# Kernel tuning notes

Hardware: AMD Instinct MI355X
Metric: run time of the kernel (lower is better)

Reference implementation:

```python
import jax, jax.numpy as jnp
import numpy as np

B, D, K, NUM_CLASSES = 8192, 512, 20, 1024
EPS = 1e-12  # torch F.normalize clamp


def setup_inputs() -> dict:
    key = jax.random.key(0)
    k1, k2 = jax.random.split(key)
    batch = jax.random.normal(k1, (B, D), dtype=jnp.float32)
    labels = jax.random.randint(k2, (B,), 0, NUM_CLASSES, dtype=jnp.int64 if jax.config.jax_enable_x64 else jnp.int32)
    return {"batch": batch, "labels": labels, "k": K}


def reference(batch, labels, k):
    # L2-normalize rows (F.normalize, p=2)
    norm = jnp.maximum(jnp.linalg.norm(batch, axis=1, keepdims=True), EPS)
    x = batch / norm
    cos = x @ x.T                                   # [B, B] cosine similarity
    min_value = cos.min() - 1.0                     # scalar, computed before diag fill
    bs = cos.shape[0]
    diag = jnp.eye(bs, dtype=bool)
    cos = jnp.where(diag, min_value, cos)           # fill_diagonal_(min_value)
    # argsort(-cos)[:, :k]  ==  top-k by similarity (self excluded via diag fill)
    top_vals, top_idx = jax.lax.top_k(cos, k)       # [B, k]
    # preds = (cos + 1)/2 gathered at neighbor indices == (top_vals + 1)/2
    preds = (top_vals + 1.0) * 0.5
    true_labels = (labels[top_idx] == labels[:, None]).astype(jnp.float32)  # [B, k]
    # nn.BCELoss with mean reduction; torch clamps each log term at -100
    logp = jnp.maximum(jnp.log(preds), -100.0)
    log1mp = jnp.maximum(jnp.log1p(-preds), -100.0)
    loss = -(true_labels * logp + (1.0 - true_labels) * log1mp)
    return loss.mean()
```

## Files before the change

kernel.cpp:

```cpp
#include <hip/hip_runtime.h>
#include <hip/hip_bf16.h>

#define NROWS 8192
#define DIM   512
#define KSEL  20
#define PANEL 1024
#define NSURV 512

typedef unsigned int u32;
typedef unsigned long long u64;
typedef short bf16x8 __attribute__((ext_vector_type(8)));
typedef float f32x4 __attribute__((ext_vector_type(4)));
typedef ushort us4 __attribute__((ext_vector_type(4)));

typedef const void __attribute__((address_space(1))) as1_void;
typedef void __attribute__((address_space(3))) as3_void;

__device__ __forceinline__ void async_ld16(const ushort* g, ushort* l) {
    __builtin_amdgcn_global_load_lds((as1_void*)g, (as3_void*)l, 16, 0, 0);
}

__device__ __forceinline__ ushort f2bf(float f) {
    u32 u = __float_as_uint(f);
    return (ushort)((u + 0x7FFFu + ((u >> 16) & 1u)) >> 16);
}

__device__ __forceinline__ u32 mono16(u32 r) {
    return r ^ (0x8000u | ((r >> 15) * 0x7FFFu));
}

__global__ __launch_bounds__(256) void k_norm(const float* __restrict__ x,
                                              ushort* __restrict__ xn) {
    int lane = threadIdx.x & 63;
    int wv   = threadIdx.x >> 6;
    int row  = blockIdx.x * 4 + wv;
    const float4* xr = (const float4*)(x + (size_t)row * DIM);
    float4 a = xr[2 * lane];
    float4 b = xr[2 * lane + 1];
    float ss = a.x*a.x + a.y*a.y + a.z*a.z + a.w*a.w
             + b.x*b.x + b.y*b.y + b.z*b.z + b.w*b.w;
    #pragma unroll
    for (int off = 32; off; off >>= 1) ss += __shfl_xor(ss, off);
    float sc = 1.0f / fmaxf(sqrtf(ss), 1e-12f);
    float v[8] = {a.x*sc, a.y*sc, a.z*sc, a.w*sc, b.x*sc, b.y*sc, b.z*sc, b.w*sc};
    union { ushort u[8]; uint4 q; } o;
    #pragma unroll
    for (int i = 0; i < 8; ++i) o.u[i] = f2bf(v[i]);
    *(uint4*)(xn + (size_t)row * DIM + lane * 8) = o.q;
}

template<bool TRI>
__global__ __launch_bounds__(256) void k_gemm(const ushort* __restrict__ xn,
                                              ushort* __restrict__ C,
                                              ushort* __restrict__ M,
                                              int row0) {
    __shared__ ushort lA[128 * 64];
    __shared__ ushort lB[128 * 64];
    int tid  = threadIdx.x;
    int lane = tid & 63, wv = tid >> 6;
    int wr = wv >> 1, wc = wv & 1;
    int q = lane >> 4, m = lane & 15;
    int bx, by;
    if (TRI) {
        int t = blockIdx.x;
        by = (int)((sqrtf(8.0f * (float)t + 1.0f) - 1.0f) * 0.5f);
        while ((by + 1) * (by + 2) / 2 <= t) ++by;
        while (by * (by + 1) / 2 > t) --by;
        bx = t - by * (by + 1) / 2;
    } else {
        bx = blockIdx.x; by = blockIdx.y;
    }
    int grow0 = row0 + by * 128;
    int gcol0 = bx * 128;
    f32x4 acc[4][4] = {};

    int lr = lane >> 3;
    int lc = lane & 7;
    for (int kc = 0; kc < 8; ++kc) {
        #pragma unroll
        for (int t = 0; t < 4; ++t) {
            int rb  = wv * 32 + t * 8;
            int r   = rb + lr;
            int fch = lc ^ (r & 7);
            async_ld16(xn + (size_t)(grow0 + r) * DIM + kc * 64 + fch * 8, &lA[rb * 64]);
            async_ld16(xn + (size_t)(gcol0 + r) * DIM + kc * 64 + fch * 8, &lB[rb * 64]);
        }
        __syncthreads();
        #pragma unroll
        for (int s = 0; s < 2; ++s) {
            bf16x8 af[4], bfr[4];
            #pragma unroll
            for (int i = 0; i < 4; ++i) {
                int ra = wr * 64 + i * 16 + m;
                af[i]  = *(const bf16x8*)&lA[ra * 64 + (((s * 4 + q) ^ (ra & 7)) * 8)];
                int rb2 = wc * 64 + i * 16 + m;
                bfr[i] = *(const bf16x8*)&lB[rb2 * 64 + (((s * 4 + q) ^ (rb2 & 7)) * 8)];
            }
            #pragma unroll
            for (int i = 0; i < 4; ++i)
                #pragma unroll
                for (int j = 0; j < 4; ++j)
                    acc[i][j] = __builtin_amdgcn_mfma_f32_16x16x32_bf16(af[i], bfr[j], acc[i][j], 0, 0, 0);
        }
        __syncthreads();
    }
    u32 cmk[4] = {0, 0, 0, 0};
    #pragma unroll
    for (int i = 0; i < 4; ++i) {
        u32 rmk[4] = {0, 0, 0, 0};
        #pragma unroll
        for (int j = 0; j < 4; ++j) {
            int c  = gcol0 + wc * 64 + j * 16 + m;
            int rb = by * 128 + wr * 64 + i * 16 + q * 4;
            ushort sv[4];
            #pragma unroll
            for (int reg = 0; reg < 4; ++reg) {
                int rl  = rb + reg;
                int grw = row0 + rl;
                ushort b = f2bf(acc[i][j][reg]);
                sv[reg] = (grw == c) ? (ushort)0xC040 : b;
                C[(size_t)rl * NROWS + c] = sv[reg];
                u32 kk = mono16((u32)sv[reg]);
                rmk[reg] = max(rmk[reg], kk);
                cmk[j]   = max(cmk[j], kk);
            }
            if (TRI && bx != by) {
                us4 pk4 = { sv[0], sv[1], sv[2], sv[3] };
                *(us4*)&C[(size_t)c * NROWS + rb] = pk4;
            }
        }
        #pragma unroll
        for (int reg = 0; reg < 4; ++reg) {
            u32 k = rmk[reg];
            k = max(k, (u32)__shfl_xor((int)k, 1));
            k = max(k, (u32)__shfl_xor((int)k, 2));
            k = max(k, (u32)__shfl_xor((int)k, 4));
            k = max(k, (u32)__shfl_xor((int)k, 8));
            if (m == 0) {
                int grw = row0 + by * 128 + wr * 64 + i * 16 + q * 4 + reg;
                M[(size_t)grw * 128 + bx * 2 + wc] = (ushort)k;
            }
        }
    }
    if (TRI && bx != by) {
        #pragma unroll
        for (int j = 0; j < 4; ++j) {
            u32 k = cmk[j];
            k = max(k, (u32)__shfl_xor((int)k, 16));
            k = max(k, (u32)__shfl_xor((int)k, 32));
            if (q == 0) {
                int gc = gcol0 + wc * 64 + j * 16 + m;
                M[(size_t)gc * 128 + by * 2 + wr] = (ushort)k;
            }
        }
    }
}

__global__ __launch_bounds__(256) void k_select(const ushort* __restrict__ C,
                                                const ushort* __restrict__ M,
                                                const int* __restrict__ labels,
                                                int row0,
                                                float* __restrict__ partials) {
    __shared__ u32 s_surv[4][NSURV];
    __shared__ u32 s_cnt[4];
    int lane = threadIdx.x & 63;
    int wv   = threadIdx.x >> 6;
    int prow = blockIdx.x * 4 + wv;
    int grow = row0 + prow;
    const ushort* rowC = C + (size_t)prow * NROWS;

    if (lane == 0) s_cnt[wv] = 0;
    __syncthreads();

    u32 pm  = *(const u32*)&M[(size_t)grow * 128 + 2 * lane];
    u32 klo = pm & 0xFFFFu, khi = pm >> 16;

    u32 T = 0;
    #pragma unroll
    for (int b = 15; b >= 0; --b) {
        u32 cand = T | (1u << b);
        int c = __popcll(__ballot(klo >= cand)) + __popcll(__ballot(khi >= cand));
        if (c >= KSEL) T = cand;
    }

    u64 rm0 = __ballot(klo >= T);
    u64 rm1 = __ballot(khi >= T);
    int nseg = __popcll(rm0) + __popcll(rm1);
    int sub = lane & 7, grp = lane >> 3;

    while (nseg > 0) {
        int ms[4] = {-1, -1, -1, -1};
        #pragma unroll
        for (int t = 0; t < 4; ++t) {
            #pragma unroll
            for (int g = 0; g < 8; ++g) {
                int seg = -1;
                if (rm0) { int b = __builtin_ctzll(rm0); seg = 2 * b;     rm0 &= rm0 - 1; }
                else if (rm1) { int b = __builtin_ctzll(rm1); seg = 2 * b + 1; rm1 &= rm1 - 1; }
                if (grp == g) ms[t] = seg;
            }
        }
        uint4 vv[4];
        #pragma unroll
        for (int t = 0; t < 4; ++t) {
            if (ms[t] >= 0) vv[t] = *(const uint4*)(rowC + ms[t] * 64 + sub * 8);
        }
        #pragma unroll
        for (int t = 0; t < 4; ++t) {
            if (ms[t] < 0) continue;
            u32 wds[4] = { vv[t].x, vv[t].y, vv[t].z, vv[t].w };
            u32 cbase = (u32)(ms[t] * 64 + sub * 8);
            #pragma unroll
            for (int h = 0; h < 4; ++h) {
                u32 w  = wds[h];
                u32 kA = mono16(w & 0xFFFFu);
                u32 kB = mono16(w >> 16);
                if (kA >= T) { u32 p = atomicAdd(&s_cnt[wv], 1u); if (p < NSURV) s_surv[wv][p] = (kA << 16) | (cbase + 2u * h); }
                if (kB >= T) { u32 p = atomicAdd(&s_cnt[wv], 1u); if (p < NSURV) s_surv[wv][p] = (kB << 16) | (cbase + 2u * h + 1u); }
            }
        }
        nseg -= 32;
    }

    u32 cnt = min(s_cnt[wv], (u32)NSURV);
    u32 g[8];
    #pragma unroll
    for (int j = 0; j < 8; ++j) {
        u32 idx = (u32)lane + (u32)j * 64u;
        g[j] = (idx < cnt) ? s_surv[wv][idx] : 0u;
    }

    u32 V = 0;
    #pragma unroll
    for (int b = 15; b >= 0; --b) {
        u32 cand = V | (1u << b);
        int c = 0;
        #pragma unroll
        for (int j = 0; j < 8; ++j)
            c += __popcll(__ballot((g[j] >> 16) >= cand));
        if (c >= KSEL) V = cand;
    }
    int cgt = 0, ceq = 0;
    #pragma unroll
    for (int j = 0; j < 8; ++j) {
        cgt += __popcll(__ballot(g[j] != 0 && (g[j] >> 16) > V));
        ceq += __popcll(__ballot(g[j] != 0 && (g[j] >> 16) == V));
    }
    int need = KSEL - cgt;
    bool all_ties = (ceq == need);

    int mylab = labels[grow];
    float loss = 0.0f;
    #pragma unroll
    for (int j = 0; j < 8; ++j) {
        u32 key = g[j] >> 16, col = g[j] & 0xFFFFu;
        if (g[j] != 0 && (key > V || (all_ties && key == V))) {
            u32 raw = (key & 0x8000u) ? (key ^ 0x8000u) : (key ^ 0xFFFFu);
            float v = __uint_as_float(raw << 16);
            float p = (v + 1.0f) * 0.5f;
            bool tm = (labels[col] == mylab);
            loss -= tm ? fmaxf(logf(p), -100.0f) : fmaxf(log1pf(-p), -100.0f);
        }
    }
    if (!all_ties) {
        for (int r = 0; r < need; ++r) {
            u32 best = 0;
            #pragma unroll
            for (int j = 0; j < 8; ++j) {
                u32 c2 = (g[j] != 0 && (g[j] >> 16) == V) ? ((g[j] & 0xFFFFu) + 1u) : 0u;
                best = max(best, c2);
            }
            #pragma unroll
            for (int off = 32; off; off >>= 1) best = max(best, (u32)__shfl_xor((int)best, off));
            #pragma unroll
            for (int j = 0; j < 8; ++j) {
                if (g[j] != 0 && (g[j] >> 16) == V && ((g[j] & 0xFFFFu) + 1u) == best) {
                    u32 col = g[j] & 0xFFFFu;
                    u32 raw = (V & 0x8000u) ? (V ^ 0x8000u) : (V ^ 0xFFFFu);
                    float v = __uint_as_float(raw << 16);
                    float p = (v + 1.0f) * 0.5f;
                    bool tm = (labels[col] == mylab);
                    loss -= tm ? fmaxf(logf(p), -100.0f) : fmaxf(log1pf(-p), -100.0f);
                    g[j] = 0;
                }
            }
        }
    }

    #pragma unroll
    for (int off = 32; off; off >>= 1) loss += __shfl_xor(loss, off);
    if (lane == 0) partials[grow] = loss;
}

__global__ __launch_bounds__(256) void k_final(const float* __restrict__ partials,
                                               float* __restrict__ out) {
    __shared__ float s[4];
    int tid = threadIdx.x, lane = tid & 63, wvi = tid >> 6;
    const float4* p4 = (const float4*)partials;
    float sum = 0.0f;
    #pragma unroll
    for (int i = 0; i < 8; ++i) {
        float4 v = p4[tid + i * 256];
        sum += v.x + v.y + v.z + v.w;
    }
    #pragma unroll
    for (int off = 32; off; off >>= 1) sum += __shfl_xor(sum, off);
    if (lane == 0) s[wvi] = sum;
    __syncthreads();
    if (tid == 0) out[0] = (s[0] + s[1] + s[2] + s[3]) * (1.0f / (float)(NROWS * KSEL));
}

extern "C" void kernel_launch(void* const* d_in, const int* in_sizes, int n_in,
                              void* d_out, int out_size, void* d_ws, size_t ws_size,
                              hipStream_t stream) {
    const float* batch  = (const float*)d_in[0];
    const int*   labels = (const int*)d_in[1];

    ushort* xn = (ushort*)d_ws;
    ushort* C  = xn + (size_t)NROWS * DIM;
    ushort* M        = (ushort*)d_in[0];
    float*  partials = (float*)((char*)d_in[0] + (4u << 20));

    size_t need_full = (size_t)NROWS * DIM * 2 + (size_t)NROWS * NROWS * 2;

    k_norm<<<NROWS / 4, 256, 0, stream>>>(batch, xn);

    if (ws_size >= need_full) {
        k_gemm<true><<<dim3(64 * 65 / 2), 256, 0, stream>>>(xn, C, M, 0);
        k_select<<<NROWS / 4, 256, 0, stream>>>(C, M, labels, 0, partials);
    } else {
        for (int p = 0; p < NROWS / PANEL; ++p) {
            k_gemm<false><<<dim3(64, PANEL / 128), 256, 0, stream>>>(xn, C, M, p * PANEL);
            k_select<<<PANEL / 4, 256, 0, stream>>>(C, M, labels, p * PANEL, partials);
        }
    }
    k_final<<<1, 256, 0, stream>>>(partials, (float*)d_out);
}
```

Before: 179.2 us.

## Stage GEMM epilogue through swizzled LDS for coalesced and transposed C stores

```diff
diff --git a/kernel.cpp b/kernel.cpp
--- a/kernel.cpp
+++ b/kernel.cpp
@@ -11,7 +11,7 @@
 typedef unsigned long long u64;
 typedef short bf16x8 __attribute__((ext_vector_type(8)));
 typedef float f32x4 __attribute__((ext_vector_type(4)));
-typedef ushort us4 __attribute__((ext_vector_type(4)));
+typedef ushort u16x2 __attribute__((ext_vector_type(2)));
 
 typedef const void __attribute__((address_space(1))) as1_void;
 typedef void __attribute__((address_space(3))) as3_void;
@@ -27,6 +27,18 @@
 
 __device__ __forceinline__ u32 mono16(u32 r) {
     return r ^ (0x8000u | ((r >> 15) * 0x7FFFu));
+}
+
+__device__ __forceinline__ u32 mkey(float f) { return mono16((u32)f2bf(f)); }
+
+__device__ __forceinline__ u32 pkmax(u32 a, u32 b) {
+    union { u32 u; u16x2 v; } x, y; x.u = a; y.u = b;
+    x.v = __builtin_elementwise_max(x.v, y.v);
+    return x.u;
+}
+
+__device__ __forceinline__ int tix(int r, int c) {
+    return r * 128 + ((c & 7) | ((((c >> 3) ^ (r >> 3)) & 15) << 3));
 }
 
 __global__ __launch_bounds__(256) void k_norm(const float* __restrict__ x,
@@ -54,8 +66,9 @@
                                               ushort* __restrict__ C,
                                               ushort* __restrict__ M,
                                               int row0) {
-    __shared__ ushort lA[128 * 64];
-    __shared__ ushort lB[128 * 64];
+    __shared__ ushort sh[2 * 128 * 64];
+    ushort* lA = sh;
+    ushort* lB = sh + 128 * 64;
     int tid  = threadIdx.x;
     int lane = tid & 63, wv = tid >> 6;
     int wr = wv >> 1, wc = wv & 1;
@@ -104,54 +117,80 @@
         }
         __syncthreads();
     }
-    u32 cmk[4] = {0, 0, 0, 0};
+
+    float cmf[4] = {-3.0f, -3.0f, -3.0f, -3.0f};
     #pragma unroll
     for (int i = 0; i < 4; ++i) {
-        u32 rmk[4] = {0, 0, 0, 0};
+        float rmf[4] = {-3.0f, -3.0f, -3.0f, -3.0f};
+        int rloc = wr * 64 + i * 16 + q * 4;
         #pragma unroll
         for (int j = 0; j < 4; ++j) {
-            int c  = gcol0 + wc * 64 + j * 16 + m;
-            int rb = by * 128 + wr * 64 + i * 16 + q * 4;
-            ushort sv[4];
+            int cl = wc * 64 + j * 16 + m;
+            int c  = gcol0 + cl;
             #pragma unroll
             for (int reg = 0; reg < 4; ++reg) {
-                int rl  = rb + reg;
-                int grw = row0 + rl;
-                ushort b = f2bf(acc[i][j][reg]);
-                sv[reg] = (grw == c) ? (ushort)0xC040 : b;
-                C[(size_t)rl * NROWS + c] = sv[reg];
-                u32 kk = mono16((u32)sv[reg]);
-                rmk[reg] = max(rmk[reg], kk);
-                cmk[j]   = max(cmk[j], kk);
-            }
-            if (TRI && bx != by) {
-                us4 pk4 = { sv[0], sv[1], sv[2], sv[3] };
-                *(us4*)&C[(size_t)c * NROWS + rb] = pk4;
-            }
-        }
-        #pragma unroll
-        for (int reg = 0; reg < 4; ++reg) {
-            u32 k = rmk[reg];
-            k = max(k, (u32)__shfl_xor((int)k, 1));
-            k = max(k, (u32)__shfl_xor((int)k, 2));
-            k = max(k, (u32)__shfl_xor((int)k, 4));
-            k = max(k, (u32)__shfl_xor((int)k, 8));
-            if (m == 0) {
-                int grw = row0 + by * 128 + wr * 64 + i * 16 + q * 4 + reg;
-                M[(size_t)grw * 128 + bx * 2 + wc] = (ushort)k;
-            }
+                int grw  = row0 + by * 128 + rloc + reg;
+                float a  = acc[i][j][reg];
+                bool dg  = (grw == c);
+                float mv = dg ? -3.0f : a;
+                rmf[reg] = fmaxf(rmf[reg], mv);
+                cmf[j]   = fmaxf(cmf[j], mv);
+                sh[tix(rloc + reg, cl)] = dg ? (ushort)0xC040 : f2bf(a);
+            }
+        }
+        u32 p01 = mkey(rmf[0]) | (mkey(rmf[1]) << 16);
+        u32 p23 = mkey(rmf[2]) | (mkey(rmf[3]) << 16);
+        #pragma unroll
+        for (int off = 1; off <= 8; off <<= 1) {
+            p01 = pkmax(p01, (u32)__shfl_xor((int)p01, off));
+            p23 = pkmax(p23, (u32)__shfl_xor((int)p23, off));
+        }
+        if (m == 0) {
+            size_t mb = (size_t)(row0 + by * 128 + rloc) * 128 + bx * 2 + wc;
+            M[mb]       = (ushort)(p01 & 0xFFFFu);
+            M[mb + 128] = (ushort)(p01 >> 16);
+            M[mb + 256] = (ushort)(p23 & 0xFFFFu);
+            M[mb + 384] = (ushort)(p23 >> 16);
         }
     }
     if (TRI && bx != by) {
-        #pragma unroll
-        for (int j = 0; j < 4; ++j) {
-            u32 k = cmk[j];
-            k = max(k, (u32)__shfl_xor((int)k, 16));
-            k = max(k, (u32)__shfl_xor((int)k, 32));
-            if (q == 0) {
-                int gc = gcol0 + wc * 64 + j * 16 + m;
-                M[(size_t)gc * 128 + by * 2 + wr] = (ushort)k;
-            }
+        u32 q01 = mkey(cmf[0]) | (mkey(cmf[1]) << 16);
+        u32 q23 = mkey(cmf[2]) | (mkey(cmf[3]) << 16);
+        q01 = pkmax(q01, (u32)__shfl_xor((int)q01, 16));
+        q01 = pkmax(q01, (u32)__shfl_xor((int)q01, 32));
+        q23 = pkmax(q23, (u32)__shfl_xor((int)q23, 16));
+        q23 = pkmax(q23, (u32)__shfl_xor((int)q23, 32));
+        if (q == 0) {
+            int gc = gcol0 + wc * 64 + m;
+            int sg = by * 2 + wr;
+            M[(size_t)(gc +  0) * 128 + sg] = (ushort)(q01 & 0xFFFFu);
+            M[(size_t)(gc + 16) * 128 + sg] = (ushort)(q01 >> 16);
+            M[(size_t)(gc + 32) * 128 + sg] = (ushort)(q23 & 0xFFFFu);
+            M[(size_t)(gc + 48) * 128 + sg] = (ushort)(q23 >> 16);
+        }
+    }
+    __syncthreads();
+
+    int tr = tid >> 4;
+    int tc = tid & 15;
+    #pragma unroll
+    for (int p = 0; p < 8; ++p) {
+        int r = p * 16 + tr;
+        uint4 v = *(const uint4*)&sh[r * 128 + (((tc ^ ((r >> 3) & 15))) << 3)];
+        *(uint4*)&C[(size_t)(by * 128 + r) * NROWS + gcol0 + tc * 8] = v;
+    }
+    if (TRI && bx != by) {
+        #pragma unroll
+        for (int p = 0; p < 8; ++p) {
+            int ct = p * 16 + tr;
+            int r8 = tc * 8;
+            u32 aw[8];
+            #pragma unroll
+            for (int k = 0; k < 8; ++k)
+                aw[k] = (u32)sh[tix(r8 + k, ct)];
+            uint4 o = { aw[0] | (aw[1] << 16), aw[2] | (aw[3] << 16),
+                        aw[4] | (aw[5] << 16), aw[6] | (aw[7] << 16) };
+            *(uint4*)&C[(size_t)(gcol0 + ct) * NROWS + by * 128 + r8] = o;
         }
     }
 }
@@ -223,65 +262,100 @@
     }
 
     u32 cnt = min(s_cnt[wv], (u32)NSURV);
-    u32 g[8];
-    #pragma unroll
-    for (int j = 0; j < 8; ++j) {
-        u32 idx = (u32)lane + (u32)j * 64u;
-        g[j] = (idx < cnt) ? s_surv[wv][idx] : 0u;
-    }
-
-    u32 V = 0;
-    #pragma unroll
-    for (int b = 15; b >= 0; --b) {
-        u32 cand = V | (1u << b);
-        int c = 0;
-        #pragma unroll
-        for (int j = 0; j < 8; ++j)
-            c += __popcll(__ballot((g[j] >> 16) >= cand));
-        if (c >= KSEL) V = cand;
-    }
-    int cgt = 0, ceq = 0;
-    #pragma unroll
-    for (int j = 0; j < 8; ++j) {
-        cgt += __popcll(__ballot(g[j] != 0 && (g[j] >> 16) > V));
-        ceq += __popcll(__ballot(g[j] != 0 && (g[j] >> 16) == V));
-    }
-    int need = KSEL - cgt;
-    bool all_ties = (ceq == need);
-
     int mylab = labels[grow];
     float loss = 0.0f;
-    #pragma unroll
-    for (int j = 0; j < 8; ++j) {
-        u32 key = g[j] >> 16, col = g[j] & 0xFFFFu;
-        if (g[j] != 0 && (key > V || (all_ties && key == V))) {
+
+    if (cnt <= 64u) {
+        u32 gg  = ((u32)lane < cnt) ? s_surv[wv][lane] : 0u;
+        u32 key = gg >> 16;
+        u32 V = 0;
+        #pragma unroll
+        for (int b = 15; b >= 0; --b) {
+            u32 cand = V | (1u << b);
+            if (__popcll(__ballot(key >= cand)) >= KSEL) V = cand;
+        }
+        int cgt  = __popcll(__ballot(key > V));
+        int ceq  = __popcll(__ballot(gg != 0 && key == V));
+        int need = KSEL - cgt;
+        bool incl;
+        if (ceq == need) {
+            incl = (gg != 0) && (key >= V);
+        } else {
+            u32 col = gg & 0xFFFFu;
+            bool tie = (gg != 0) && (key == V);
+            u32 Cv = 0;
+            #pragma unroll
+            for (int b = 15; b >= 0; --b) {
+                u32 cand2 = Cv | (1u << b);
+                if (__popcll(__ballot(tie && col >= cand2)) >= need) Cv = cand2;
+            }
+            incl = (key > V) || (tie && col >= Cv);
+        }
+        if (incl) {
+            u32 col = gg & 0xFFFFu;
             u32 raw = (key & 0x8000u) ? (key ^ 0x8000u) : (key ^ 0xFFFFu);
             float v = __uint_as_float(raw << 16);
             float p = (v + 1.0f) * 0.5f;
             bool tm = (labels[col] == mylab);
             loss -= tm ? fmaxf(logf(p), -100.0f) : fmaxf(log1pf(-p), -100.0f);
         }
-    }
-    if (!all_ties) {
-        for (int r = 0; r < need; ++r) {
-            u32 best = 0;
-            #pragma unroll
-            for (int j = 0; j < 8; ++j) {
-                u32 c2 = (g[j] != 0 && (g[j] >> 16) == V) ? ((g[j] & 0xFFFFu) + 1u) : 0u;
-                best = max(best, c2);
-            }
-            #pragma unroll
-            for (int off = 32; off; off >>= 1) best = max(best, (u32)__shfl_xor((int)best, off));
-            #pragma unroll
-            for (int j = 0; j < 8; ++j) {
-                if (g[j] != 0 && (g[j] >> 16) == V && ((g[j] & 0xFFFFu) + 1u) == best) {
-                    u32 col = g[j] & 0xFFFFu;
-                    u32 raw = (V & 0x8000u) ? (V ^ 0x8000u) : (V ^ 0xFFFFu);
-                    float v = __uint_as_float(raw << 16);
-                    float p = (v + 1.0f) * 0.5f;
-                    bool tm = (labels[col] == mylab);
-                    loss -= tm ? fmaxf(logf(p), -100.0f) : fmaxf(log1pf(-p), -100.0f);
-                    g[j] = 0;
+    } else {
+        u32 g[8];
+        #pragma unroll
+        for (int j = 0; j < 8; ++j) {
+            u32 idx = (u32)lane + (u32)j * 64u;
+            g[j] = (idx < cnt) ? s_surv[wv][idx] : 0u;
+        }
+        u32 V = 0;
+        #pragma unroll
+        for (int b = 15; b >= 0; --b) {
+            u32 cand = V | (1u << b);
+            int c = 0;
+            #pragma unroll
+            for (int j = 0; j < 8; ++j)
+                c += __popcll(__ballot((g[j] >> 16) >= cand));
+            if (c >= KSEL) V = cand;
+        }
+        int cgt = 0, ceq = 0;
+        #pragma unroll
+        for (int j = 0; j < 8; ++j) {
+            cgt += __popcll(__ballot(g[j] != 0 && (g[j] >> 16) > V));
+            ceq += __popcll(__ballot(g[j] != 0 && (g[j] >> 16) == V));
+        }
+        int need = KSEL - cgt;
+        bool all_ties = (ceq == need);
+        #pragma unroll
+        for (int j = 0; j < 8; ++j) {
+            u32 key = g[j] >> 16, col = g[j] & 0xFFFFu;
+            if (g[j] != 0 && (key > V || (all_ties && key == V))) {
+                u32 raw = (key & 0x8000u) ? (key ^ 0x8000u) : (key ^ 0xFFFFu);
+                float v = __uint_as_float(raw << 16);
+                float p = (v + 1.0f) * 0.5f;
+                bool tm = (labels[col] == mylab);
+                loss -= tm ? fmaxf(logf(p), -100.0f) : fmaxf(log1pf(-p), -100.0f);
+            }
+        }
+        if (!all_ties) {
+            for (int r = 0; r < need; ++r) {
+                u32 best = 0;
+                #pragma unroll
+                for (int j = 0; j < 8; ++j) {
+                    u32 c2 = (g[j] != 0 && (g[j] >> 16) == V) ? ((g[j] & 0xFFFFu) + 1u) : 0u;
+                    best = max(best, c2);
+                }
+                #pragma unroll
+                for (int off = 32; off; off >>= 1) best = max(best, (u32)__shfl_xor((int)best, off));
+                #pragma unroll
+                for (int j = 0; j < 8; ++j) {
+                    if (g[j] != 0 && (g[j] >> 16) == V && ((g[j] & 0xFFFFu) + 1u) == best) {
+                        u32 col = g[j] & 0xFFFFu;
+                        u32 raw = (V & 0x8000u) ? (V ^ 0x8000u) : (V ^ 0xFFFFu);
+                        float v = __uint_as_float(raw << 16);
+                        float p = (v + 1.0f) * 0.5f;
+                        bool tm = (labels[col] == mylab);
+                        loss -= tm ? fmaxf(logf(p), -100.0f) : fmaxf(log1pf(-p), -100.0f);
+                        g[j] = 0;
+                    }
                 }
             }
         }
```

New measurement: 166.7 us. -7.0%, faster.
